# Performance work log

Hardware: AMD Instinct MI355X
Metric: run time of the kernel (lower is better)

The kernel has to match this reference:

```python
import jax, jax.numpy as jnp
import numpy as np

D = 4096
N_HEAD = 32
KV_HEAD = 8
GS = D * KV_HEAD // N_HEAD  # 1024, kv projection width
B, S = 1, 2048


def setup_inputs() -> dict:
    key = jax.random.key(0)
    ks = jax.random.split(key, 10)
    sc = 0.02
    return {
        "x": jax.random.normal(ks[0], (B, S, D), dtype=jnp.float32),
        "y": jax.random.normal(ks[1], (B, S, D), dtype=jnp.float32),
        "Wq": jax.random.normal(ks[2], (D, D), dtype=jnp.float32) * sc,
        "bq": jax.random.normal(ks[3], (D,), dtype=jnp.float32) * sc,
        "Wk": jax.random.normal(ks[4], (D, GS), dtype=jnp.float32) * sc,
        "bk": jax.random.normal(ks[5], (GS,), dtype=jnp.float32) * sc,
        "Wv": jax.random.normal(ks[6], (D, GS), dtype=jnp.float32) * sc,
        "bv": jax.random.normal(ks[7], (GS,), dtype=jnp.float32) * sc,
        "Wo": jax.random.normal(ks[8], (D, D), dtype=jnp.float32) * sc,
        "bo": jax.random.normal(ks[9], (D,), dtype=jnp.float32) * sc,
        "n_head": N_HEAD,
        "kv_head": KV_HEAD,
    }


def reference(x, y, Wq, bq, Wk, bk, Wv, bv, Wo, bo, n_head, kv_head):
    b, s, d = x.shape
    hd = d // n_head              # per-head dim
    gvs = hd // 2                 # complex pairs per head (group_vector_size)
    q = (x @ Wq + bq).reshape(b, s, n_head, hd)
    k = (y @ Wk + bk).reshape(b, s, kv_head, hd)
    v = (y @ Wv + bv).reshape(b, s, kv_head, hd)

    # RoPE: phi = 1/5000**(i/gvs); angle[p, i] = phi[i] * p  (matrix.T in torch)
    phi = 1.0 / (5000.0 ** (jnp.arange(gvs, dtype=jnp.float32) / gvs))
    ang = jnp.arange(s, dtype=jnp.float32)[:, None] * phi[None, :]  # [S, gvs]
    cos = jnp.cos(ang)[None, :, None, :]  # [1,S,1,gvs]
    sin = jnp.sin(ang)[None, :, None, :]

    def rope(t):
        # interleaved pairs (t[...,2i], t[...,2i+1]) form complex numbers
        tr, ti = t[..., 0::2], t[..., 1::2]
        ro = tr * cos - ti * sin
        io = tr * sin + ti * cos
        return jnp.stack([ro, io], axis=-1).reshape(t.shape)

    q = rope(q)
    k = rope(k)

    # GQA: head h uses kv head h // (n_head // kv_head) -> repeat kv heads
    module = n_head // kv_head
    k = jnp.repeat(k, module, axis=2)  # [B,S,H,hd]
    v = jnp.repeat(v, module, axis=2)

    scores = jnp.einsum("bqhd,bkhd->bhqk", q, k) / jnp.sqrt(jnp.float32(hd))
    causal = jnp.tril(jnp.ones((s, s), dtype=bool))
    scores = jnp.where(causal[None, None], scores, -jnp.inf)
    attn = jax.nn.softmax(scores, axis=-1)
    out = jnp.einsum("bhqk,bkhd->bqhd", attn, v).reshape(b, s, d)
    return out @ Wo + bo
```

## Files before the change

### kernel.cpp

```cpp
#include <hip/hip_runtime.h>
#include <hip/hip_bf16.h>

typedef unsigned int uint32;
typedef unsigned short ushort16;
typedef __attribute__((ext_vector_type(8))) __bf16 bf16x8;
typedef __attribute__((ext_vector_type(4))) float f32x4;

__device__ __forceinline__ ushort16 f2bf(float f) {
    uint32 u = __float_as_uint(f);
    u += 0x7fff + ((u >> 16) & 1);
    return (ushort16)(u >> 16);
}
__device__ __forceinline__ uint32 pack2rn(float a, float b) {
    uint32 ua = __float_as_uint(a) + 0x8000u;
    uint32 ub = __float_as_uint(b) + 0x8000u;
    return __builtin_amdgcn_perm(ub, ua, 0x07060302);
}
__device__ __forceinline__ float blo(uint32 u) { return __uint_as_float(u << 16); }
__device__ __forceinline__ float bhi(uint32 u) { return __uint_as_float(u & 0xffff0000u); }

__device__ __forceinline__ void storeC(float v, float* p) { *p = v; }
__device__ __forceinline__ void storeC(float v, ushort16* p) { *p = f2bf(v); }

__device__ __forceinline__ void gload_lds16(const void* g, void* l) {
    __builtin_amdgcn_global_load_lds(
        (const __attribute__((address_space(1))) unsigned int*)g,
        (__attribute__((address_space(3))) unsigned int*)l, 16, 0, 0);
}

__global__ __launch_bounds__(256) void prep_kernel(
    const float* __restrict__ x, const float* __restrict__ y,
    const float* __restrict__ Wq, const float* __restrict__ Wk,
    const float* __restrict__ Wv, const float* __restrict__ Wo,
    ushort16* __restrict__ xb, ushort16* __restrict__ yb,
    ushort16* __restrict__ Wqt, ushort16* __restrict__ Wkvt,
    ushort16* __restrict__ Wot)
{
    __shared__ float tile[64][65];
    const int b = blockIdx.x;
    if (b < 8192) {
        const int n8 = 1048576;
        int idx = b * 256 + threadIdx.x;
        const float* S = (idx < n8) ? x : y;
        ushort16*    D = (idx < n8) ? xb : yb;
        int i = (idx < n8) ? idx : idx - n8;
        float4 a = ((const float4*)S)[2 * i];
        float4 c = ((const float4*)S)[2 * i + 1];
        uint4 u;
        u.x = pack2rn(a.x, a.y); u.y = pack2rn(a.z, a.w);
        u.z = pack2rn(c.x, c.y); u.w = pack2rn(c.z, c.w);
        ((uint4*)D)[i] = u;
        return;
    }
    int t = b - 8192;
    int kblk = t & 63, sel = t >> 6;
    const float* W; ushort16* Wt; int N, n0;
    if (sel < 64)      { W = Wq; Wt = Wqt;  N = 4096; n0 = sel * 64; }
    else if (sel < 80) { W = Wk; Wt = Wkvt; N = 1024; n0 = (sel - 64) * 64; }
    else if (sel < 96) { W = Wv; Wt = Wkvt + (size_t)1024 * 4096; N = 1024; n0 = (sel - 80) * 64; }
    else               { W = Wo; Wt = Wot;  N = 4096; n0 = (sel - 96) * 64; }
    const int k0 = kblk * 64;
#pragma unroll
    for (int it = 0; it < 16; ++it) {
        int idx = threadIdx.x + it * 256;
        int r = idx >> 6, c = idx & 63;
        tile[r][c] = W[(size_t)(k0 + r) * N + n0 + c];
    }
    __syncthreads();
#pragma unroll
    for (int it = 0; it < 8; ++it) {
        int idx = threadIdx.x + it * 256;
        int nr = idx >> 5, kp = idx & 31;
        uint32 u = pack2rn(tile[2 * kp][nr], tile[2 * kp + 1][nr]);
        *(uint32*)&Wt[(size_t)(n0 + nr) * 4096 + k0 + 2 * kp] = u;
    }
}

__global__ __launch_bounds__(256) void gemm_qkv(
    const ushort16* __restrict__ xb, const ushort16* __restrict__ yb,
    const ushort16* __restrict__ Wqt, const ushort16* __restrict__ Wkvt,
    const float* __restrict__ bq, const float* __restrict__ bk,
    const float* __restrict__ bv, float* __restrict__ Q,
    ushort16* __restrict__ KVb)
{
    __shared__ __align__(16) ushort16 As[128 * 64];
    __shared__ __align__(16) ushort16 Bs[128 * 64];

    const bool isQ = (blockIdx.x < 32);
    const ushort16* A = isQ ? xb : yb;
    const ushort16* B = isQ ? Wqt : Wkvt;
    const int gn0 = (isQ ? (int)blockIdx.x : (int)blockIdx.x - 32) * 128;
    const int gm0 = blockIdx.y * 128;
    const int K = 4096;

    const int tid  = threadIdx.x;
    const int lane = tid & 63, wave = tid >> 6;
    const int quad = lane >> 4, m16 = lane & 15;
    const int wm = (wave >> 1) * 64, wn = (wave & 1) * 64;

    f32x4 acc[4][4];
#pragma unroll
    for (int i = 0; i < 4; ++i)
#pragma unroll
        for (int j = 0; j < 4; ++j) acc[i][j] = (f32x4){0.f, 0.f, 0.f, 0.f};

    const int rl = lane >> 3, cl = lane & 7;
    const int clog = cl ^ (rl & 7);
    const ushort16* Ag = A + (size_t)(gm0 + wave * 32 + rl) * K + clog * 8;
    const ushort16* Bg = B + (size_t)(gn0 + wave * 32 + rl) * K + clog * 8;
    char* AsW = (char*)As + wave * 4096;
    char* BsW = (char*)Bs + wave * 4096;

    for (int k0 = 0; k0 < K; k0 += 64) {
        __syncthreads();
#pragma unroll
        for (int i = 0; i < 4; ++i) {
            gload_lds16(Ag + (size_t)(8 * i) * K, AsW + i * 1024);
            gload_lds16(Bg + (size_t)(8 * i) * K, BsW + i * 1024);
        }
        Ag += 64; Bg += 64;
        __syncthreads();

#pragma unroll
        for (int s = 0; s < 2; ++s) {
            bf16x8 aF[4], bF[4];
            const int cr = s * 4 + quad;
#pragma unroll
            for (int i = 0; i < 4; ++i) {
                int r = wm + i * 16 + m16;
                aF[i] = *(const bf16x8*)&As[r * 64 + ((cr ^ (r & 7)) * 8)];
                int n = wn + i * 16 + m16;
                bF[i] = *(const bf16x8*)&Bs[n * 64 + ((cr ^ (n & 7)) * 8)];
            }
            __builtin_amdgcn_s_setprio(1);
#pragma unroll
            for (int i = 0; i < 4; ++i)
#pragma unroll
                for (int j = 0; j < 4; ++j)
                    acc[i][j] = __builtin_amdgcn_mfma_f32_16x16x32_bf16(
                        aF[i], bF[j], acc[i][j], 0, 0, 0);
            __builtin_amdgcn_s_setprio(0);
        }
    }

#pragma unroll
    for (int j = 0; j < 4; ++j) {
        int col = gn0 + wn + j * 16 + m16;
        float bb = isQ ? bq[col] : ((col < 1024) ? bk[col] : bv[col - 1024]);
#pragma unroll
        for (int i = 0; i < 4; ++i) {
            int row0 = gm0 + wm + i * 16 + quad * 4;
#pragma unroll
            for (int r = 0; r < 4; ++r) {
                float v = acc[i][j][r] + bb;
                if (isQ) Q[(size_t)(row0 + r) * 4096 + col] = v;
                else     KVb[(size_t)(row0 + r) * 2048 + col] = f2bf(v);
            }
        }
    }
}

template <typename OutT>
__global__ __launch_bounds__(256) void gemm_mfma(
    const ushort16* __restrict__ A, const ushort16* __restrict__ B,
    const float* __restrict__ b1, OutT* __restrict__ C, int N, int K)
{
    __shared__ __align__(16) ushort16 As[128 * 64];
    __shared__ __align__(16) ushort16 Bs[128 * 64];

    const int tid  = threadIdx.x;
    const int lane = tid & 63, wave = tid >> 6;
    const int quad = lane >> 4, m16 = lane & 15;
    const int wm = (wave >> 1) * 64, wn = (wave & 1) * 64;
    const int gm0 = blockIdx.y * 128, gn0 = blockIdx.x * 128;

    f32x4 acc[4][4];
#pragma unroll
    for (int i = 0; i < 4; ++i)
#pragma unroll
        for (int j = 0; j < 4; ++j) acc[i][j] = (f32x4){0.f, 0.f, 0.f, 0.f};

    const int rl = lane >> 3, cl = lane & 7;
    const int clog = cl ^ (rl & 7);
    const ushort16* Ag = A + (size_t)(gm0 + wave * 32 + rl) * K + clog * 8;
    const ushort16* Bg = B + (size_t)(gn0 + wave * 32 + rl) * K + clog * 8;
    char* AsW = (char*)As + wave * 4096;
    char* BsW = (char*)Bs + wave * 4096;

    for (int k0 = 0; k0 < K; k0 += 64) {
        __syncthreads();
#pragma unroll
        for (int i = 0; i < 4; ++i) {
            gload_lds16(Ag + (size_t)(8 * i) * K, AsW + i * 1024);
            gload_lds16(Bg + (size_t)(8 * i) * K, BsW + i * 1024);
        }
        Ag += 64; Bg += 64;
        __syncthreads();

#pragma unroll
        for (int s = 0; s < 2; ++s) {
            bf16x8 aF[4], bF[4];
            const int cr = s * 4 + quad;
#pragma unroll
            for (int i = 0; i < 4; ++i) {
                int r = wm + i * 16 + m16;
                aF[i] = *(const bf16x8*)&As[r * 64 + ((cr ^ (r & 7)) * 8)];
                int n = wn + i * 16 + m16;
                bF[i] = *(const bf16x8*)&Bs[n * 64 + ((cr ^ (n & 7)) * 8)];
            }
            __builtin_amdgcn_s_setprio(1);
#pragma unroll
            for (int i = 0; i < 4; ++i)
#pragma unroll
                for (int j = 0; j < 4; ++j)
                    acc[i][j] = __builtin_amdgcn_mfma_f32_16x16x32_bf16(
                        aF[i], bF[j], acc[i][j], 0, 0, 0);
            __builtin_amdgcn_s_setprio(0);
        }
    }

#pragma unroll
    for (int j = 0; j < 4; ++j) {
        int col = gn0 + wn + j * 16 + m16;
        float bb = b1[col];
#pragma unroll
        for (int i = 0; i < 4; ++i) {
            int row0 = gm0 + wm + i * 16 + quad * 4;
#pragma unroll
            for (int r = 0; r < 4; ++r)
                storeC(acc[i][j][r] + bb, C + (size_t)(row0 + r) * N + col);
        }
    }
}

__global__ __launch_bounds__(256) void rope_vt_kernel(
    const float* __restrict__ T, ushort16* __restrict__ Qb,
    ushort16* __restrict__ KVb, ushort16* __restrict__ Vt)
{
    __shared__ ushort16 tile[64][66];
    const int b = blockIdx.x;
    if (b < 16384) {
        int idx = b * 256 + threadIdx.x;
        int i   = idx & 63;
        int rem = idx >> 6;
        int s   = rem >> 5;
        float inv = powf(5000.0f, -(float)i / 64.0f);
        float ang = (float)s * inv;
        float cs = cosf(ang), sn = sinf(ang);
        const float sc = 0.08838834764831845f * 1.4426950408889634f;
        size_t base = (size_t)rem * 128 + 2 * i;
        float tr = T[base], ti = T[base + 1];
        *(uint32*)&Qb[base] = pack2rn((tr * cs - ti * sn) * sc,
                                      (tr * sn + ti * cs) * sc);
        return;
    }
    if (b < 20480) {
        int idx = (b - 16384) * 256 + threadIdx.x;
        int i   = idx & 63;
        int rem = idx >> 6;
        int s   = rem >> 3, h = rem & 7;
        float inv = powf(5000.0f, -(float)i / 64.0f);
        float ang = (float)s * inv;
        float cs = cosf(ang), sn = sinf(ang);
        uint32* p = (uint32*)&KVb[(size_t)s * 2048 + h * 128 + 2 * i];
        uint32 u = *p;
        float tr = blo(u), ti = bhi(u);
        *p = pack2rn(tr * cs - ti * sn, tr * sn + ti * cs);
        return;
    }
    int t = b - 20480;
    int s0 = (t >> 4) * 64, d0 = (t & 15) * 64;
#pragma unroll
    for (int it = 0; it < 2; ++it) {
        int i = threadIdx.x + it * 256;
        int r = i >> 3, c = (i & 7) * 8;
        *(uint4*)&tile[r][c] = *(const uint4*)&KVb[(size_t)(s0 + r) * 2048 + 1024 + d0 + c];
    }
    __syncthreads();
#pragma unroll
    for (int it = 0; it < 2; ++it) {
        int i = threadIdx.x + it * 256;
        int dr = i >> 3, sc = (i & 7) * 8;
        uint32 w[4];
#pragma unroll
        for (int q = 0; q < 4; ++q)
            w[q] = (uint32)tile[sc + 2 * q][dr] | ((uint32)tile[sc + 2 * q + 1][dr] << 16);
        *(uint4*)&Vt[(size_t)(d0 + dr) * 2048 + s0 + sc] = *(uint4*)w;
    }
}

__global__ __launch_bounds__(256) void flash_attn_kernel(
    const ushort16* __restrict__ Qb, const ushort16* __restrict__ KVb,
    const ushort16* __restrict__ Vtg, ushort16* __restrict__ O)
{
    __shared__ __align__(16) ushort16 Kb[2][64 * 128];
    __shared__ __align__(16) ushort16 Vs[128 * 64];
    __shared__ __align__(16) ushort16 Ps[64 * 64];

    const int tid  = threadIdx.x;
    const int lane = tid & 63, wave = tid >> 6;
    const int quad = lane >> 4, m16 = lane & 15;
    const int h = (int)blockIdx.y, kvh = h >> 2;

    const ushort16* Kbase = KVb + kvh * 128;
    const ushort16* Vbase = Vtg + (size_t)(kvh * 128) * 2048;

    const int rK = lane >> 4;
    const ushort16* pKe = Kbase + (size_t)(wave * 16 + rK) * 2048
                        + (((lane & 15) ^ rK) * 8);
    const ushort16* pKo = Kbase + (size_t)(wave * 16 + 4 + rK) * 2048
                        + (((lane & 15) ^ (4 + rK)) * 8);
    const int rV = lane >> 3;
    const ushort16* pV  = Vbase + (size_t)(wave * 32 + rV) * 2048
                        + (((lane & 7) ^ rV) * 8);
    char* ldsK0 = (char*)&Kb[0][0] + wave * 4096;
    char* ldsK1 = (char*)&Kb[1][0] + wave * 4096;
    char* ldsV  = (char*)&Vs[0]    + wave * 4096;

#define STAGE_K(dst, kk) do {                                   \
        const ushort16* _s0 = pKe + (size_t)(kk) * 2048;        \
        const ushort16* _s1 = pKo + (size_t)(kk) * 2048;        \
        gload_lds16(_s0,            (dst));                     \
        gload_lds16(_s1,            (dst) + 1024);              \
        gload_lds16(_s0 + 8 * 2048, (dst) + 2048);              \
        gload_lds16(_s1 + 8 * 2048, (dst) + 3072);              \
    } while (0)
#define STAGE_V(kk) do {                                        \
        const ushort16* _sv = pV + (kk);                        \
        gload_lds16(_sv,             ldsV);                     \
        gload_lds16(_sv +  8 * 2048, ldsV + 1024);              \
        gload_lds16(_sv + 16 * 2048, ldsV + 2048);              \
        gload_lds16(_sv + 24 * 2048, ldsV + 3072);              \
    } while (0)

    for (int pass = 0; pass < 2; ++pass) {
        const int qi = pass ? (int)blockIdx.x : 31 - (int)blockIdx.x;
        const int q0 = qi * 64;

        bf16x8 qa[4];
        {
            const ushort16* qp = Qb + (size_t)(q0 + wave * 16 + m16) * 4096
                               + h * 128 + quad * 8;
#pragma unroll
            for (int ks = 0; ks < 4; ++ks)
                qa[ks] = *(const bf16x8*)(qp + ks * 32);
        }

        f32x4 acc_o[8];
#pragma unroll
        for (int t = 0; t < 8; ++t) acc_o[t] = (f32x4){0.f, 0.f, 0.f, 0.f};
        float m_i[4], l_i[4];
#pragma unroll
        for (int r = 0; r < 4; ++r) { m_i[r] = -1e30f; l_i[r] = 0.f; }

        int cur = 0;
        STAGE_K(ldsK0, 0);

        for (int k0 = 0; k0 <= q0; k0 += 64) {
            __syncthreads();

            STAGE_V(k0);
            const bool pre = (k0 + 64 <= q0);
            if (pre) STAGE_K(cur ? ldsK0 : ldsK1, k0 + 64);

            const ushort16* Kcur = &Kb[cur][0];

            f32x4 sacc[4];
#pragma unroll
            for (int j = 0; j < 4; ++j) sacc[j] = (f32x4){0.f, 0.f, 0.f, 0.f};
            __builtin_amdgcn_s_setprio(1);
#pragma unroll
            for (int ks = 0; ks < 4; ++ks) {
#pragma unroll
                for (int j = 0; j < 4; ++j) {
                    int n = j * 16 + m16;
                    bf16x8 kb = *(const bf16x8*)&Kcur[n * 128 + (((ks * 4 + quad) ^ (n & 7)) * 8)];
                    sacc[j] = __builtin_amdgcn_mfma_f32_16x16x32_bf16(qa[ks], kb, sacc[j], 0, 0, 0);
                }
            }
            __builtin_amdgcn_s_setprio(0);

            if (k0 == q0) {
                int qr = wave * 16 + quad * 4;
#pragma unroll
                for (int j = 0; j < 4; ++j) {
                    int kvl = j * 16 + m16;
#pragma unroll
                    for (int r = 0; r < 4; ++r)
                        if (kvl > qr + r) sacc[j][r] = -1e30f;
                }
            }

#pragma unroll
            for (int r = 0; r < 4; ++r) {
                float rm = fmaxf(fmaxf(sacc[0][r], sacc[1][r]), fmaxf(sacc[2][r], sacc[3][r]));
                rm = fmaxf(rm, __shfl_xor(rm, 1));
                rm = fmaxf(rm, __shfl_xor(rm, 2));
                rm = fmaxf(rm, __shfl_xor(rm, 4));
                rm = fmaxf(rm, __shfl_xor(rm, 8));
                float mnew = fmaxf(m_i[r], rm);
                float al = exp2f(m_i[r] - mnew);
                float rs = 0.f;
#pragma unroll
                for (int j = 0; j < 4; ++j) {
                    float pv = exp2f(sacc[j][r] - mnew);
                    sacc[j][r] = pv;
                    rs += pv;
                }
                rs += __shfl_xor(rs, 1);
                rs += __shfl_xor(rs, 2);
                rs += __shfl_xor(rs, 4);
                rs += __shfl_xor(rs, 8);
                l_i[r] = l_i[r] * al + rs;
                m_i[r] = mnew;
                int q = wave * 16 + quad * 4 + r;
#pragma unroll
                for (int j = 0; j < 4; ++j) {
                    int kv = j * 16 + m16;
                    Ps[q * 64 + (((kv >> 3) ^ (q & 7)) * 8) + (kv & 7)] = f2bf(sacc[j][r]);
                }
#pragma unroll
                for (int t = 0; t < 8; ++t) acc_o[t][r] *= al;
            }

            if (pre) { asm volatile("s_waitcnt vmcnt(4)" ::: "memory"); }
            else     { asm volatile("s_waitcnt vmcnt(0)" ::: "memory"); }
            __builtin_amdgcn_sched_barrier(0);
            __builtin_amdgcn_s_barrier();

            int qrow = wave * 16 + m16;
#pragma unroll
            for (int ks2 = 0; ks2 < 2; ++ks2) {
                bf16x8 pa = *(const bf16x8*)&Ps[qrow * 64 + (((ks2 * 4 + quad) ^ (qrow & 7)) * 8)];
                __builtin_amdgcn_s_setprio(1);
#pragma unroll
                for (int t = 0; t < 8; ++t) {
                    int d = t * 16 + m16;
                    bf16x8 vb = *(const bf16x8*)&Vs[d * 64 + (((ks2 * 4 + quad) ^ (d & 7)) * 8)];
                    acc_o[t] = __builtin_amdgcn_mfma_f32_16x16x32_bf16(pa, vb, acc_o[t], 0, 0, 0);
                }
                __builtin_amdgcn_s_setprio(0);
            }
            cur ^= 1;
        }

        ushort16* op = O + (size_t)(q0 + wave * 16 + quad * 4) * 4096 + h * 128 + m16;
#pragma unroll
        for (int r = 0; r < 4; ++r) {
            float inv = 1.0f / l_i[r];
#pragma unroll
            for (int t = 0; t < 8; ++t)
                op[(size_t)r * 4096 + t * 16] = f2bf(acc_o[t][r] * inv);
        }
    }
#undef STAGE_K
#undef STAGE_V
}

extern "C" void kernel_launch(void* const* d_in, const int* in_sizes, int n_in,
                              void* d_out, int out_size, void* d_ws, size_t ws_size,
                              hipStream_t stream)
{
    const float* x  = (const float*)d_in[0];
    const float* y  = (const float*)d_in[1];
    const float* Wq = (const float*)d_in[2];
    const float* bq = (const float*)d_in[3];
    const float* Wk = (const float*)d_in[4];
    const float* bk = (const float*)d_in[5];
    const float* Wv = (const float*)d_in[6];
    const float* bv = (const float*)d_in[7];
    const float* Wo = (const float*)d_in[8];
    const float* bo = (const float*)d_in[9];
    float* out = (float*)d_out;

    const size_t MB = 1024 * 1024;

    char* ws = (char*)d_ws;
    ushort16* xb   = (ushort16*)(ws);
    ushort16* yb   = (ushort16*)(ws + 16 * MB);
    ushort16* Wqt  = (ushort16*)(ws + 32 * MB);
    ushort16* Wkvt = (ushort16*)(ws + 64 * MB);
    ushort16* Wot  = (ushort16*)(ws + 80 * MB);
    ushort16* KVb  = (ushort16*)(ws + 112 * MB);
    ushort16* Vtg  = (ushort16*)(ws + 120 * MB);
    ushort16* Qb   = xb;
    ushort16* Ao   = yb;
    float*    Q    = out;

    prep_kernel<<<18432, 256, 0, stream>>>(x, y, Wq, Wk, Wv, Wo,
                                           xb, yb, Wqt, Wkvt, Wot);

    gemm_qkv<<<dim3(48, 16), 256, 0, stream>>>(
        xb, yb, Wqt, Wkvt, bq, bk, bv, Q, KVb);

    rope_vt_kernel<<<20992, 256, 0, stream>>>(Q, Qb, KVb, Vtg);

    flash_attn_kernel<<<dim3(16, 32), 256, 0, stream>>>(Qb, KVb, Vtg, Ao);

    gemm_mfma<float><<<dim3(32, 16), 256, 0, stream>>>(
        Ao, Wot, bo, out, 4096, 4096);
}
```

Before: 574.1 us.

## Fuse RoPE into QKV GEMM epilogue and skip softmax rescale when max unchanged

Moves the RoPE rotation and softmax scaling for Q and K into the QKV GEMM epilogue. Pairs are exchanged by lane shuffles and written as packed bf16, so the float32 Q round-trip and the separate rope pass go away. The remaining kernel only transposes V. In flash attention, the running-max rescale of the accumulators is skipped when no row max grows, and the P tile is padded to a 72-element stride. Using fast __sinf/__cosf on angles up to 2047 can lose accuracy, and Q now aliases the output buffer as bf16.

```diff
diff --git a/kernel.cpp b/kernel.cpp
--- a/kernel.cpp
+++ b/kernel.cpp
@@ -27,6 +27,8 @@
         (const __attribute__((address_space(1))) unsigned int*)g,
         (__attribute__((address_space(3))) unsigned int*)l, 16, 0, 0);
 }
+
+#define ROPE_NEGSTEP (-0.19199550593046019f)
 
 __global__ __launch_bounds__(256) void prep_kernel(
     const float* __restrict__ x, const float* __restrict__ y,
@@ -80,7 +82,7 @@
     const ushort16* __restrict__ xb, const ushort16* __restrict__ yb,
     const ushort16* __restrict__ Wqt, const ushort16* __restrict__ Wkvt,
     const float* __restrict__ bq, const float* __restrict__ bk,
-    const float* __restrict__ bv, float* __restrict__ Q,
+    const float* __restrict__ bv, ushort16* __restrict__ Qb,
     ushort16* __restrict__ KVb)
 {
     __shared__ __align__(16) ushort16 As[128 * 64];
@@ -143,18 +145,73 @@
         }
     }
 
-#pragma unroll
-    for (int j = 0; j < 4; ++j) {
-        int col = gn0 + wn + j * 16 + m16;
-        float bb = isQ ? bq[col] : ((col < 1024) ? bk[col] : bv[col - 1024]);
-#pragma unroll
-        for (int i = 0; i < 4; ++i) {
-            int row0 = gm0 + wm + i * 16 + quad * 4;
-#pragma unroll
-            for (int r = 0; r < 4; ++r) {
-                float v = acc[i][j][r] + bb;
-                if (isQ) Q[(size_t)(row0 + r) * 4096 + col] = v;
-                else     KVb[(size_t)(row0 + r) * 2048 + col] = f2bf(v);
+    if (isQ) {
+        const float sc = 0.08838834764831845f * 1.4426950408889634f;
+#pragma unroll
+        for (int j = 0; j < 4; ++j) {
+            int col = gn0 + wn + j * 16 + m16;
+            float bb = bq[col];
+            int ip = (col & 127) >> 1;
+            float inv = exp2f((float)ip * ROPE_NEGSTEP);
+#pragma unroll
+            for (int i = 0; i < 4; ++i) {
+                int row0 = gm0 + wm + i * 16 + quad * 4;
+#pragma unroll
+                for (int r = 0; r < 4; ++r) {
+                    int s = row0 + r;
+                    float v = acc[i][j][r] + bb;
+                    float pv = __shfl_xor(v, 1);
+                    float ang = (float)s * inv;
+                    float sn = __sinf(ang), cs = __cosf(ang);
+                    float o = (lane & 1) ? (pv * sn + v * cs)
+                                         : (v * cs - pv * sn);
+                    o *= sc;
+                    float po = __shfl_xor(o, 1);
+                    if (!(lane & 1))
+                        *(uint32*)&Qb[(size_t)s * 4096 + col] = pack2rn(o, po);
+                }
+            }
+        }
+    } else if (gn0 < 1024) {
+#pragma unroll
+        for (int j = 0; j < 4; ++j) {
+            int col = gn0 + wn + j * 16 + m16;
+            float bb = bk[col];
+            int ip = (col & 127) >> 1;
+            float inv = exp2f((float)ip * ROPE_NEGSTEP);
+#pragma unroll
+            for (int i = 0; i < 4; ++i) {
+                int row0 = gm0 + wm + i * 16 + quad * 4;
+#pragma unroll
+                for (int r = 0; r < 4; ++r) {
+                    int s = row0 + r;
+                    float v = acc[i][j][r] + bb;
+                    float pv = __shfl_xor(v, 1);
+                    float ang = (float)s * inv;
+                    float sn = __sinf(ang), cs = __cosf(ang);
+                    float o = (lane & 1) ? (pv * sn + v * cs)
+                                         : (v * cs - pv * sn);
+                    float po = __shfl_xor(o, 1);
+                    if (!(lane & 1))
+                        *(uint32*)&KVb[(size_t)s * 2048 + col] = pack2rn(o, po);
+                }
+            }
+        }
+    } else {
+#pragma unroll
+        for (int j = 0; j < 4; ++j) {
+            int col = gn0 + wn + j * 16 + m16;
+            float bb = bv[col - 1024];
+#pragma unroll
+            for (int i = 0; i < 4; ++i) {
+                int row0 = gm0 + wm + i * 16 + quad * 4;
+#pragma unroll
+                for (int r = 0; r < 4; ++r) {
+                    float v = acc[i][j][r] + bb;
+                    float pv = __shfl_xor(v, 1);
+                    if (!(lane & 1))
+                        *(uint32*)&KVb[(size_t)(row0 + r) * 2048 + col] = pack2rn(v, pv);
+                }
             }
         }
     }
@@ -233,42 +290,11 @@
     }
 }
 
-__global__ __launch_bounds__(256) void rope_vt_kernel(
-    const float* __restrict__ T, ushort16* __restrict__ Qb,
-    ushort16* __restrict__ KVb, ushort16* __restrict__ Vt)
+__global__ __launch_bounds__(256) void vtrans_kernel(
+    const ushort16* __restrict__ KVb, ushort16* __restrict__ Vt)
 {
     __shared__ ushort16 tile[64][66];
-    const int b = blockIdx.x;
-    if (b < 16384) {
-        int idx = b * 256 + threadIdx.x;
-        int i   = idx & 63;
-        int rem = idx >> 6;
-        int s   = rem >> 5;
-        float inv = powf(5000.0f, -(float)i / 64.0f);
-        float ang = (float)s * inv;
-        float cs = cosf(ang), sn = sinf(ang);
-        const float sc = 0.08838834764831845f * 1.4426950408889634f;
-        size_t base = (size_t)rem * 128 + 2 * i;
-        float tr = T[base], ti = T[base + 1];
-        *(uint32*)&Qb[base] = pack2rn((tr * cs - ti * sn) * sc,
-                                      (tr * sn + ti * cs) * sc);
-        return;
-    }
-    if (b < 20480) {
-        int idx = (b - 16384) * 256 + threadIdx.x;
-        int i   = idx & 63;
-        int rem = idx >> 6;
-        int s   = rem >> 3, h = rem & 7;
-        float inv = powf(5000.0f, -(float)i / 64.0f);
-        float ang = (float)s * inv;
-        float cs = cosf(ang), sn = sinf(ang);
-        uint32* p = (uint32*)&KVb[(size_t)s * 2048 + h * 128 + 2 * i];
-        uint32 u = *p;
-        float tr = blo(u), ti = bhi(u);
-        *p = pack2rn(tr * cs - ti * sn, tr * sn + ti * cs);
-        return;
-    }
-    int t = b - 20480;
+    int t = blockIdx.x;
     int s0 = (t >> 4) * 64, d0 = (t & 15) * 64;
 #pragma unroll
     for (int it = 0; it < 2; ++it) {
@@ -295,7 +321,7 @@
 {
     __shared__ __align__(16) ushort16 Kb[2][64 * 128];
     __shared__ __align__(16) ushort16 Vs[128 * 64];
-    __shared__ __align__(16) ushort16 Ps[64 * 64];
+    __shared__ __align__(16) ushort16 Ps[64 * 72];
 
     const int tid  = threadIdx.x;
     const int lane = tid & 63, wave = tid >> 6;
@@ -391,19 +417,35 @@
                 }
             }
 
+            float rm[4];
 #pragma unroll
             for (int r = 0; r < 4; ++r) {
-                float rm = fmaxf(fmaxf(sacc[0][r], sacc[1][r]), fmaxf(sacc[2][r], sacc[3][r]));
-                rm = fmaxf(rm, __shfl_xor(rm, 1));
-                rm = fmaxf(rm, __shfl_xor(rm, 2));
-                rm = fmaxf(rm, __shfl_xor(rm, 4));
-                rm = fmaxf(rm, __shfl_xor(rm, 8));
-                float mnew = fmaxf(m_i[r], rm);
-                float al = exp2f(m_i[r] - mnew);
+                float v = fmaxf(fmaxf(sacc[0][r], sacc[1][r]), fmaxf(sacc[2][r], sacc[3][r]));
+                v = fmaxf(v, __shfl_xor(v, 1));
+                v = fmaxf(v, __shfl_xor(v, 2));
+                v = fmaxf(v, __shfl_xor(v, 4));
+                v = fmaxf(v, __shfl_xor(v, 8));
+                rm[r] = v;
+            }
+            int ok = (rm[0] <= m_i[0]) & (rm[1] <= m_i[1]) &
+                     (rm[2] <= m_i[2]) & (rm[3] <= m_i[3]);
+            if (!__all(ok)) {
+#pragma unroll
+                for (int r = 0; r < 4; ++r) {
+                    float mnew = fmaxf(m_i[r], rm[r]);
+                    float al = exp2f(m_i[r] - mnew);
+                    l_i[r] *= al;
+                    m_i[r] = mnew;
+#pragma unroll
+                    for (int t = 0; t < 8; ++t) acc_o[t][r] *= al;
+                }
+            }
+#pragma unroll
+            for (int r = 0; r < 4; ++r) {
                 float rs = 0.f;
 #pragma unroll
                 for (int j = 0; j < 4; ++j) {
-                    float pv = exp2f(sacc[j][r] - mnew);
+                    float pv = exp2f(sacc[j][r] - m_i[r]);
                     sacc[j][r] = pv;
                     rs += pv;
                 }
@@ -411,16 +453,13 @@
                 rs += __shfl_xor(rs, 2);
                 rs += __shfl_xor(rs, 4);
                 rs += __shfl_xor(rs, 8);
-                l_i[r] = l_i[r] * al + rs;
-                m_i[r] = mnew;
+                l_i[r] += rs;
                 int q = wave * 16 + quad * 4 + r;
 #pragma unroll
                 for (int j = 0; j < 4; ++j) {
                     int kv = j * 16 + m16;
-                    Ps[q * 64 + (((kv >> 3) ^ (q & 7)) * 8) + (kv & 7)] = f2bf(sacc[j][r]);
-                }
-#pragma unroll
-                for (int t = 0; t < 8; ++t) acc_o[t][r] *= al;
+                    Ps[q * 72 + (((kv >> 3) ^ (q & 7)) * 8) + (kv & 7)] = f2bf(sacc[j][r]);
+                }
             }
 
             if (pre) { asm volatile("s_waitcnt vmcnt(4)" ::: "memory"); }
@@ -431,7 +470,7 @@
             int qrow = wave * 16 + m16;
 #pragma unroll
             for (int ks2 = 0; ks2 < 2; ++ks2) {
-                bf16x8 pa = *(const bf16x8*)&Ps[qrow * 64 + (((ks2 * 4 + quad) ^ (qrow & 7)) * 8)];
+                bf16x8 pa = *(const bf16x8*)&Ps[qrow * 72 + (((ks2 * 4 + quad) ^ (qrow & 7)) * 8)];
                 __builtin_amdgcn_s_setprio(1);
 #pragma unroll
                 for (int t = 0; t < 8; ++t) {
@@ -483,17 +522,16 @@
     ushort16* Wot  = (ushort16*)(ws + 80 * MB);
     ushort16* KVb  = (ushort16*)(ws + 112 * MB);
     ushort16* Vtg  = (ushort16*)(ws + 120 * MB);
-    ushort16* Qb   = xb;
     ushort16* Ao   = yb;
-    float*    Q    = out;
+    ushort16* Qb   = (ushort16*)out;
 
     prep_kernel<<<18432, 256, 0, stream>>>(x, y, Wq, Wk, Wv, Wo,
                                            xb, yb, Wqt, Wkvt, Wot);
 
     gemm_qkv<<<dim3(48, 16), 256, 0, stream>>>(
-        xb, yb, Wqt, Wkvt, bq, bk, bv, Q, KVb);
-
-    rope_vt_kernel<<<20992, 256, 0, stream>>>(Q, Qb, KVb, Vtg);
+        xb, yb, Wqt, Wkvt, bq, bk, bv, Qb, KVb);
+
+    vtrans_kernel<<<512, 256, 0, stream>>>(KVb, Vtg);
 
     flash_attn_kernel<<<dim3(16, 32), 256, 0, stream>>>(Qb, KVb, Vtg, Ao);
 
```

Result: slower. 618.4 us (+7.7%).

## Fuse Q RoPE into attention load, skip rescale when max unchanged, pad P

Applied to the files above, without the earlier changes.

Q RoPE and scaling move out of the separate rope kernel and into the attention kernel's Q fragment load. Each attention block now reads fp32 Q and rotates it in registers, which removes a 16M-element elementwise pass and its bf16 round trip through memory. The online softmax now skips the accumulator rescale when no row max grows across the wave. The P tile in LDS is padded to a 72-element stride, and RoPE uses exp2f and fast __sinf/__cosf, which may lose accuracy for large angles.

```diff
diff --git a/kernel.cpp b/kernel.cpp
--- a/kernel.cpp
+++ b/kernel.cpp
@@ -26,6 +26,16 @@
     __builtin_amdgcn_global_load_lds(
         (const __attribute__((address_space(1))) unsigned int*)g,
         (__attribute__((address_space(3))) unsigned int*)l, 16, 0, 0);
+}
+
+#define ROPE_NEGSTEP (-0.19199550593046019f)
+
+__device__ __forceinline__ uint32 rope_pack(float tr, float ti, int ip, int s,
+                                            float sc) {
+    float inv = exp2f((float)ip * ROPE_NEGSTEP);
+    float ang = (float)s * inv;
+    float sn = __sinf(ang), cs = __cosf(ang);
+    return pack2rn((tr * cs - ti * sn) * sc, (tr * sn + ti * cs) * sc);
 }
 
 __global__ __launch_bounds__(256) void prep_kernel(
@@ -233,42 +243,26 @@
     }
 }
 
-__global__ __launch_bounds__(256) void rope_vt_kernel(
-    const float* __restrict__ T, ushort16* __restrict__ Qb,
+__global__ __launch_bounds__(256) void ropek_vt_kernel(
     ushort16* __restrict__ KVb, ushort16* __restrict__ Vt)
 {
     __shared__ ushort16 tile[64][66];
     const int b = blockIdx.x;
-    if (b < 16384) {
+    if (b < 4096) {
         int idx = b * 256 + threadIdx.x;
         int i   = idx & 63;
         int rem = idx >> 6;
-        int s   = rem >> 5;
-        float inv = powf(5000.0f, -(float)i / 64.0f);
+        int s   = rem >> 3, h = rem & 7;
+        float inv = exp2f((float)i * ROPE_NEGSTEP);
         float ang = (float)s * inv;
-        float cs = cosf(ang), sn = sinf(ang);
-        const float sc = 0.08838834764831845f * 1.4426950408889634f;
-        size_t base = (size_t)rem * 128 + 2 * i;
-        float tr = T[base], ti = T[base + 1];
-        *(uint32*)&Qb[base] = pack2rn((tr * cs - ti * sn) * sc,
-                                      (tr * sn + ti * cs) * sc);
-        return;
-    }
-    if (b < 20480) {
-        int idx = (b - 16384) * 256 + threadIdx.x;
-        int i   = idx & 63;
-        int rem = idx >> 6;
-        int s   = rem >> 3, h = rem & 7;
-        float inv = powf(5000.0f, -(float)i / 64.0f);
-        float ang = (float)s * inv;
-        float cs = cosf(ang), sn = sinf(ang);
+        float cs = __cosf(ang), sn = __sinf(ang);
         uint32* p = (uint32*)&KVb[(size_t)s * 2048 + h * 128 + 2 * i];
         uint32 u = *p;
         float tr = blo(u), ti = bhi(u);
         *p = pack2rn(tr * cs - ti * sn, tr * sn + ti * cs);
         return;
     }
-    int t = b - 20480;
+    int t = b - 4096;
     int s0 = (t >> 4) * 64, d0 = (t & 15) * 64;
 #pragma unroll
     for (int it = 0; it < 2; ++it) {
@@ -290,12 +284,12 @@
 }
 
 __global__ __launch_bounds__(256) void flash_attn_kernel(
-    const ushort16* __restrict__ Qb, const ushort16* __restrict__ KVb,
+    const float* __restrict__ Qf, const ushort16* __restrict__ KVb,
     const ushort16* __restrict__ Vtg, ushort16* __restrict__ O)
 {
     __shared__ __align__(16) ushort16 Kb[2][64 * 128];
     __shared__ __align__(16) ushort16 Vs[128 * 64];
-    __shared__ __align__(16) ushort16 Ps[64 * 64];
+    __shared__ __align__(16) ushort16 Ps[64 * 72];
 
     const int tid  = threadIdx.x;
     const int lane = tid & 63, wave = tid >> 6;
@@ -336,14 +330,24 @@
     for (int pass = 0; pass < 2; ++pass) {
         const int qi = pass ? (int)blockIdx.x : 31 - (int)blockIdx.x;
         const int q0 = qi * 64;
-
+        const int srow = q0 + wave * 16 + m16;
+
+        const float sc = 0.08838834764831845f * 1.4426950408889634f;
         bf16x8 qa[4];
         {
-            const ushort16* qp = Qb + (size_t)(q0 + wave * 16 + m16) * 4096
-                               + h * 128 + quad * 8;
-#pragma unroll
-            for (int ks = 0; ks < 4; ++ks)
-                qa[ks] = *(const bf16x8*)(qp + ks * 32);
+            const float* qp = Qf + (size_t)srow * 4096 + h * 128 + quad * 8;
+#pragma unroll
+            for (int ks = 0; ks < 4; ++ks) {
+                float4 a = *(const float4*)(qp + ks * 32);
+                float4 b = *(const float4*)(qp + ks * 32 + 4);
+                int ip0 = quad * 4 + ks * 16;
+                uint4 u;
+                u.x = rope_pack(a.x, a.y, ip0 + 0, srow, sc);
+                u.y = rope_pack(a.z, a.w, ip0 + 1, srow, sc);
+                u.z = rope_pack(b.x, b.y, ip0 + 2, srow, sc);
+                u.w = rope_pack(b.z, b.w, ip0 + 3, srow, sc);
+                qa[ks] = *(bf16x8*)&u;
+            }
         }
 
         f32x4 acc_o[8];
@@ -391,19 +395,35 @@
                 }
             }
 
+            float rm[4];
 #pragma unroll
             for (int r = 0; r < 4; ++r) {
-                float rm = fmaxf(fmaxf(sacc[0][r], sacc[1][r]), fmaxf(sacc[2][r], sacc[3][r]));
-                rm = fmaxf(rm, __shfl_xor(rm, 1));
-                rm = fmaxf(rm, __shfl_xor(rm, 2));
-                rm = fmaxf(rm, __shfl_xor(rm, 4));
-                rm = fmaxf(rm, __shfl_xor(rm, 8));
-                float mnew = fmaxf(m_i[r], rm);
-                float al = exp2f(m_i[r] - mnew);
+                float v = fmaxf(fmaxf(sacc[0][r], sacc[1][r]), fmaxf(sacc[2][r], sacc[3][r]));
+                v = fmaxf(v, __shfl_xor(v, 1));
+                v = fmaxf(v, __shfl_xor(v, 2));
+                v = fmaxf(v, __shfl_xor(v, 4));
+                v = fmaxf(v, __shfl_xor(v, 8));
+                rm[r] = v;
+            }
+            int ok = (rm[0] <= m_i[0]) & (rm[1] <= m_i[1]) &
+                     (rm[2] <= m_i[2]) & (rm[3] <= m_i[3]);
+            if (!__all(ok)) {
+#pragma unroll
+                for (int r = 0; r < 4; ++r) {
+                    float mnew = fmaxf(m_i[r], rm[r]);
+                    float al = exp2f(m_i[r] - mnew);
+                    l_i[r] *= al;
+                    m_i[r] = mnew;
+#pragma unroll
+                    for (int t = 0; t < 8; ++t) acc_o[t][r] *= al;
+                }
+            }
+#pragma unroll
+            for (int r = 0; r < 4; ++r) {
                 float rs = 0.f;
 #pragma unroll
                 for (int j = 0; j < 4; ++j) {
-                    float pv = exp2f(sacc[j][r] - mnew);
+                    float pv = exp2f(sacc[j][r] - m_i[r]);
                     sacc[j][r] = pv;
                     rs += pv;
                 }
@@ -411,16 +431,13 @@
                 rs += __shfl_xor(rs, 2);
                 rs += __shfl_xor(rs, 4);
                 rs += __shfl_xor(rs, 8);
-                l_i[r] = l_i[r] * al + rs;
-                m_i[r] = mnew;
+                l_i[r] += rs;
                 int q = wave * 16 + quad * 4 + r;
 #pragma unroll
                 for (int j = 0; j < 4; ++j) {
                     int kv = j * 16 + m16;
-                    Ps[q * 64 + (((kv >> 3) ^ (q & 7)) * 8) + (kv & 7)] = f2bf(sacc[j][r]);
+                    Ps[q * 72 + (((kv >> 3) ^ (q & 7)) * 8) + (kv & 7)] = f2bf(sacc[j][r]);
                 }
-#pragma unroll
-                for (int t = 0; t < 8; ++t) acc_o[t][r] *= al;
             }
 
             if (pre) { asm volatile("s_waitcnt vmcnt(4)" ::: "memory"); }
@@ -431,7 +448,7 @@
             int qrow = wave * 16 + m16;
 #pragma unroll
             for (int ks2 = 0; ks2 < 2; ++ks2) {
-                bf16x8 pa = *(const bf16x8*)&Ps[qrow * 64 + (((ks2 * 4 + quad) ^ (qrow & 7)) * 8)];
+                bf16x8 pa = *(const bf16x8*)&Ps[qrow * 72 + (((ks2 * 4 + quad) ^ (qrow & 7)) * 8)];
                 __builtin_amdgcn_s_setprio(1);
 #pragma unroll
                 for (int t = 0; t < 8; ++t) {
@@ -483,7 +500,6 @@
     ushort16* Wot  = (ushort16*)(ws + 80 * MB);
     ushort16* KVb  = (ushort16*)(ws + 112 * MB);
     ushort16* Vtg  = (ushort16*)(ws + 120 * MB);
-    ushort16* Qb   = xb;
     ushort16* Ao   = yb;
     float*    Q    = out;
 
@@ -493,9 +509,9 @@
     gemm_qkv<<<dim3(48, 16), 256, 0, stream>>>(
         xb, yb, Wqt, Wkvt, bq, bk, bv, Q, KVb);
 
-    rope_vt_kernel<<<20992, 256, 0, stream>>>(Q, Qb, KVb, Vtg);
-
-    flash_attn_kernel<<<dim3(16, 32), 256, 0, stream>>>(Qb, KVb, Vtg, Ao);
+    ropek_vt_kernel<<<4608, 256, 0, stream>>>(KVb, Vtg);
+
+    flash_attn_kernel<<<dim3(16, 32), 256, 0, stream>>>(Q, KVb, Vtg, Ao);
 
     gemm_mfma<float><<<dim3(32, 16), 256, 0, stream>>>(
         Ao, Wot, bo, out, 4096, 4096);
```

Result: no change. 567.9 us (-1.1%).
